# Kernel tuning notes

Hardware: AMD Instinct MI355X
Metric: run time of the kernel (lower is better)

The kernel has to match this reference:

```python
import jax, jax.numpy as jnp
import numpy as np

N_NODES = 50000
N_EDGES = 1250000
IN_CH = 64
HID = 64
N_CLASSES = 10
N_GRAPHS = 128


def _xavier(key, shape):
    fan_out, fan_in = shape
    limit = np.sqrt(6.0 / (fan_in + fan_out))
    return jax.random.uniform(key, shape, jnp.float32, -limit, limit)


def setup_inputs() -> dict:
    key = jax.random.key(0)
    ks = jax.random.split(key, 12)
    x = jax.random.normal(ks[0], (N_NODES, IN_CH), jnp.float32)
    edge_index = jax.random.randint(ks[1], (2, N_EDGES), 0, N_NODES, jnp.int64)
    batch = jnp.sort(jax.random.randint(ks[2], (N_NODES,), 0, N_GRAPHS, jnp.int64))
    return {
        "x": x,
        "edge_index": edge_index,
        "batch": batch,
        # GraphConv i: lin_rel (weight+bias) applied to aggregated neighbors,
        # lin_root (no bias) applied to self features. Weights are [out, in].
        "W1_rel": _xavier(ks[3], (HID, IN_CH)), "b1": jnp.zeros((HID,), jnp.float32),
        "W1_root": _xavier(ks[4], (HID, IN_CH)),
        "W2_rel": _xavier(ks[5], (HID, HID)), "b2": jnp.zeros((HID,), jnp.float32),
        "W2_root": _xavier(ks[6], (HID, HID)),
        "W3_rel": _xavier(ks[7], (HID, HID)), "b3": jnp.zeros((HID,), jnp.float32),
        "W3_root": _xavier(ks[8], (HID, HID)),
        "W_lin": _xavier(ks[9], (N_CLASSES, HID)), "b_lin": jnp.zeros((N_CLASSES,), jnp.float32),
    }


def _graph_conv(x, src, dst, W_rel, b, W_root):
    # sum-aggregate neighbor features: gather at src, scatter-add at dst
    agg = jax.ops.segment_sum(x[src], dst, num_segments=N_NODES)  # [N, F]
    return agg @ W_rel.T + b + x @ W_root.T


def reference(x, edge_index, batch, W1_rel, b1, W1_root, W2_rel, b2, W2_root,
              W3_rel, b3, W3_root, W_lin, b_lin):
    src, dst = edge_index[0], edge_index[1]
    h = jax.nn.relu(_graph_conv(x, src, dst, W1_rel, b1, W1_root))
    h = jax.nn.relu(_graph_conv(h, src, dst, W2_rel, b2, W2_root))
    h = _graph_conv(h, src, dst, W3_rel, b3, W3_root)
    # global mean pool over graphs
    sums = jax.ops.segment_sum(h, batch, num_segments=N_GRAPHS)        # [G, HID]
    counts = jax.ops.segment_sum(jnp.ones((h.shape[0],), h.dtype), batch,
                                 num_segments=N_GRAPHS)
    pooled = sums / jnp.maximum(counts, 1.0)[:, None]
    out = pooled @ W_lin.T + b_lin  # dropout inactive in eval mode
    return (pooled, out)
```

## Files before the change

kernel.cpp:

```cpp
#include <hip/hip_runtime.h>

#define N_NODES   50000
#define HID       64
#define N_GRAPHS  128
#define N_CLASSES 10
#define NP        196
#define EPA       8192
#define PCAP      8192

typedef __attribute__((ext_vector_type(8))) short short8;
typedef __attribute__((ext_vector_type(4))) float f32x4;

__device__ __forceinline__ unsigned bf16rne(float f) {
    unsigned u = __float_as_uint(f);
    return (u + 0x7fffu + ((u >> 16) & 1u)) >> 16;
}
__device__ __forceinline__ unsigned pack_bf16x2(float lo, float hi) {
    return bf16rne(lo) | (bf16rne(hi) << 16);
}



__global__ void cvt_kernel(const float* __restrict__ x, unsigned short* __restrict__ xb,
                           int* __restrict__ gcursor) {
    if (blockIdx.x == 0 && threadIdx.x < NP) gcursor[threadIdx.x] = 0;
    int i = blockIdx.x * blockDim.x + threadIdx.x;
    if (i < N_NODES * 16) {
        float4 v = ((const float4*)x)[i];
        uint2 o;
        o.x = pack_bf16x2(v.x, v.y);
        o.y = pack_bf16x2(v.z, v.w);
        ((uint2*)xb)[i] = o;
    }
}


__global__ __launch_bounds__(256) void bucket_kernel(
    const int* __restrict__ src, const int* __restrict__ dst,
    int* __restrict__ gcursor, unsigned* __restrict__ packed, int E) {
    __shared__ int hist[NP], scp[NP], base[NP], cnt2[NP];
    __shared__ int sc[256];
    __shared__ unsigned stag[EPA];
    const int t = threadIdx.x;
    const int e0 = blockIdx.x * EPA;
    const int e1 = min(e0 + EPA, E);
    for (int i = t; i < NP; i += 256) { hist[i] = 0; cnt2[i] = 0; }
    __syncthreads();
    for (int e = e0 + t; e < e1; e += 256)
        atomicAdd(&hist[dst[e] >> 8], 1);
    __syncthreads();
    sc[t] = (t < NP) ? hist[t] : 0;
    __syncthreads();
    for (int off = 1; off < 256; off <<= 1) {
        int add = (t >= off) ? sc[t - off] : 0;
        __syncthreads();
        sc[t] += add;
        __syncthreads();
    }
    if (t < NP) {
        scp[t] = sc[t] - hist[t];
        if (hist[t] > 0) base[t] = atomicAdd(&gcursor[t], hist[t]);
    }
    __syncthreads();
    for (int e = e0 + t; e < e1; e += 256) {
        int d = dst[e], s = src[e];
        int p = d >> 8;
        int idx = scp[p] + atomicAdd(&cnt2[p], 1);
        stag[idx] = (unsigned)s | ((unsigned)(d & 255) << 16) | ((unsigned)p << 24);
    }
    __syncthreads();
    const int n = e1 - e0;
    for (int i = t; i < n; i += 256) {
        unsigned v = stag[i];
        int p = v >> 24;
        packed[(size_t)p * PCAP + base[p] + (i - scp[p])] = v & 0x00FFFFFFu;
    }
}

__global__ __launch_bounds__(256) void build_kernel(
    const unsigned* __restrict__ packed, const int* __restrict__ gcursor,
    int* __restrict__ offsets, unsigned short* __restrict__ csr,
    int* __restrict__ sums_zero) {
    __shared__ int hist[256], lofs[256], cnt[256], sc[256], gv[256];
    __shared__ unsigned short lcsr[PCAP];
    const int p = blockIdx.x, t = threadIdx.x;

    if (p == 0) {
        for (int i = t; i < N_GRAPHS * 64; i += 256) sums_zero[i] = 0;
    }

    int v = (t < NP) ? gcursor[t] : 0;
    sc[t] = v; gv[t] = v;
    __syncthreads();
    for (int off = 1; off < 256; off <<= 1) {
        int add = (t >= off) ? sc[t - off] : 0;
        __syncthreads();
        sc[t] += add;
        __syncthreads();
    }
    const int pb = sc[p] - gv[p];
    const int ne = gv[p];
    if (p == NP - 1 && t == 0) offsets[N_NODES] = sc[NP - 1];
    __syncthreads();

    const unsigned* mypk = packed + (size_t)p * PCAP;
    hist[t] = 0; cnt[t] = 0;
    __syncthreads();
    for (int i = t; i < ne; i += 256)
        atomicAdd(&hist[(mypk[i] >> 16) & 255], 1);
    __syncthreads();
    sc[t] = hist[t];
    __syncthreads();
    for (int off = 1; off < 256; off <<= 1) {
        int add = (t >= off) ? sc[t - off] : 0;
        __syncthreads();
        sc[t] += add;
        __syncthreads();
    }
    lofs[t] = sc[t] - hist[t];
    int node = p * 256 + t;
    if (node < N_NODES) offsets[node] = pb + lofs[t];
    __syncthreads();
    for (int i = t; i < ne; i += 256) {
        unsigned vv = mypk[i];
        int dl = (vv >> 16) & 255;
        int slot = lofs[dl] + atomicAdd(&cnt[dl], 1);
        lcsr[slot] = (unsigned short)(vv & 0xFFFFu);
    }
    __syncthreads();
    for (int i = t; i < ne; i += 256) csr[pb + i] = lcsr[i];
}


__global__ __launch_bounds__(256) void gather_kernel(
    const unsigned short* __restrict__ hin,
    const int* __restrict__ offsets, const unsigned short* __restrict__ csr_src,
    unsigned short* __restrict__ agg) {
    const int w = threadIdx.x >> 6, lane = threadIdx.x & 63;
    const int rg = lane >> 3;
    const int cg = lane & 7;
    const int n = blockIdx.x * 4 + w;
    const int beg = offsets[n], end = offsets[n + 1];

    float acc[8] = {0.f, 0.f, 0.f, 0.f, 0.f, 0.f, 0.f, 0.f};
    for (int base = beg; base < end; base += 64) {
        int cnt = min(64, end - base);
        int sidx = (base + lane < end) ? (int)csr_src[base + lane] : 0;
        for (int kb = 0; kb < cnt; kb += 32) {
            uint4 u[4];
#pragma unroll
            for (int p = 0; p < 4; ++p) {
                int e = kb + 8 * p + rg;
                int r = __shfl(sidx, e);
                if (e < cnt)
                    u[p] = *((const uint4*)(hin + (size_t)r * 64) + cg);
                else
                    u[p] = make_uint4(0u, 0u, 0u, 0u);
            }
#pragma unroll
            for (int p = 0; p < 4; ++p) {
                acc[0] += __uint_as_float(u[p].x << 16);
                acc[1] += __uint_as_float(u[p].x & 0xffff0000u);
                acc[2] += __uint_as_float(u[p].y << 16);
                acc[3] += __uint_as_float(u[p].y & 0xffff0000u);
                acc[4] += __uint_as_float(u[p].z << 16);
                acc[5] += __uint_as_float(u[p].z & 0xffff0000u);
                acc[6] += __uint_as_float(u[p].w << 16);
                acc[7] += __uint_as_float(u[p].w & 0xffff0000u);
            }
        }
    }
#pragma unroll
    for (int m = 8; m <= 32; m <<= 1)
#pragma unroll
        for (int j = 0; j < 8; ++j)
            acc[j] += __shfl_xor(acc[j], m);
    if (rg == 0) {
        uint4 o;
        o.x = pack_bf16x2(acc[0], acc[1]);
        o.y = pack_bf16x2(acc[2], acc[3]);
        o.z = pack_bf16x2(acc[4], acc[5]);
        o.w = pack_bf16x2(acc[6], acc[7]);
        *((uint4*)(agg + (size_t)n * 64) + cg) = o;
    }
}


template <int RELU, int POOL>
__global__ __launch_bounds__(256) void linear_kernel(
    const unsigned short* __restrict__ agg,
    const unsigned short* __restrict__ hin,
    const float* __restrict__ Wrel, const float* __restrict__ bias,
    const float* __restrict__ Wroot, unsigned short* __restrict__ hout,
    const int* __restrict__ batch, float* __restrict__ sums) {
    const int tid = threadIdx.x;
    const int w = tid >> 6, lane = tid & 63;
    const int q = lane >> 4, c = lane & 15;
    const int g0 = (blockIdx.x * 4 + w) * 16;
    if (g0 >= N_NODES) return;

    short8 brel[4][2], broot[4][2];
    float biasv[4];
#pragma unroll
    for (int t = 0; t < 4; ++t) {
        int o = t * 16 + c;
        biasv[t] = bias[o];
#pragma unroll
        for (int s = 0; s < 2; ++s) {
            const float4* pr = (const float4*)(Wrel  + o * 64 + s * 32 + q * 8);
            const float4* po = (const float4*)(Wroot + o * 64 + s * 32 + q * 8);
            float4 r0 = pr[0], r1 = pr[1], z0 = po[0], z1 = po[1];
            short8 rr, zz;
            rr[0] = (short)bf16rne(r0.x); rr[1] = (short)bf16rne(r0.y);
            rr[2] = (short)bf16rne(r0.z); rr[3] = (short)bf16rne(r0.w);
            rr[4] = (short)bf16rne(r1.x); rr[5] = (short)bf16rne(r1.y);
            rr[6] = (short)bf16rne(r1.z); rr[7] = (short)bf16rne(r1.w);
            zz[0] = (short)bf16rne(z0.x); zz[1] = (short)bf16rne(z0.y);
            zz[2] = (short)bf16rne(z0.z); zz[3] = (short)bf16rne(z0.w);
            zz[4] = (short)bf16rne(z1.x); zz[5] = (short)bf16rne(z1.y);
            zz[6] = (short)bf16rne(z1.z); zz[7] = (short)bf16rne(z1.w);
            brel[t][s] = rr; broot[t][s] = zz;
        }
    }

    const int na = min(g0 + c, N_NODES - 1);
    short8 a_agg[2], a_x[2];
#pragma unroll
    for (int s = 0; s < 2; ++s) {
        a_agg[s] = *(const short8*)(agg + (size_t)na * 64 + s * 32 + q * 8);
        a_x[s]   = *(const short8*)(hin + (size_t)na * 64 + s * 32 + q * 8);
    }

    f32x4 acc4[4];
#pragma unroll
    for (int t = 0; t < 4; ++t) {
        f32x4 a0 = {biasv[t], biasv[t], biasv[t], biasv[t]};
        a0 = __builtin_amdgcn_mfma_f32_16x16x32_bf16(a_agg[0], brel[t][0], a0, 0, 0, 0);
        a0 = __builtin_amdgcn_mfma_f32_16x16x32_bf16(a_agg[1], brel[t][1], a0, 0, 0, 0);
        a0 = __builtin_amdgcn_mfma_f32_16x16x32_bf16(a_x[0],  broot[t][0], a0, 0, 0, 0);
        a0 = __builtin_amdgcn_mfma_f32_16x16x32_bf16(a_x[1],  broot[t][1], a0, 0, 0, 0);
        acc4[t] = a0;
    }

    if (POOL) {
        int b0 = batch[g0], b15 = batch[g0 + 15];
        if (b0 == b15) {
#pragma unroll
            for (int t = 0; t < 4; ++t) {
                float s = acc4[t][0] + acc4[t][1] + acc4[t][2] + acc4[t][3];
                s += __shfl_xor(s, 16);
                s += __shfl_xor(s, 32);
                if (q == 0) atomicAdd(&sums[b0 * 64 + t * 16 + c], s);
            }
        } else {
#pragma unroll
            for (int r = 0; r < 4; ++r) {
                int bq = batch[g0 + q * 4 + r];
#pragma unroll
                for (int t = 0; t < 4; ++t)
                    atomicAdd(&sums[bq * 64 + t * 16 + c], acc4[t][r]);
            }
        }
    } else {
        __shared__ unsigned short outT[4][16][72];
#pragma unroll
        for (int t = 0; t < 4; ++t)
#pragma unroll
            for (int r = 0; r < 4; ++r) {
                float v = acc4[t][r];
                if (RELU) v = fmaxf(v, 0.f);
                outT[w][q * 4 + r][t * 16 + c] = (unsigned short)bf16rne(v);
            }
#pragma unroll
        for (int it = 0; it < 2; ++it) {
            int row = it * 8 + (lane >> 3);
            int ch = (lane & 7) * 8;
            int n = g0 + row;
            if (n < N_NODES) {
                short8 v = *(const short8*)&outT[w][row][ch];
                *(short8*)(hout + (size_t)n * 64 + ch) = v;
            }
        }
    }
}


__global__ void final_kernel(const float* __restrict__ sums, const int* __restrict__ batch,
                             const float* __restrict__ Wlin, const float* __restrict__ blin,
                             float* __restrict__ out) {
    __shared__ float pl[64];
    int g = blockIdx.x, lane = threadIdx.x;
    int lo = 0, hi = N_NODES;
    while (lo < hi) { int m = (lo + hi) >> 1; if (batch[m] < g) lo = m + 1; else hi = m; }
    int s0 = lo;
    lo = 0; hi = N_NODES;
    while (lo < hi) { int m = (lo + hi) >> 1; if (batch[m] < g + 1) lo = m + 1; else hi = m; }
    float cdiv = fmaxf((float)(lo - s0), 1.0f);
    float p = sums[g * 64 + lane] / cdiv;
    out[g * 64 + lane] = p;
    pl[lane] = p;
    __syncthreads();
    if (lane < N_CLASSES) {
        float o = blin[lane];
#pragma unroll
        for (int k = 0; k < 64; ++k) o += pl[k] * Wlin[lane * 64 + k];
        out[N_GRAPHS * 64 + g * N_CLASSES + lane] = o;
    }
}


extern "C" void kernel_launch(void* const* d_in, const int* in_sizes, int n_in,
                              void* d_out, int out_size, void* d_ws, size_t ws_size,
                              hipStream_t stream) {
    const float* x     = (const float*)d_in[0];
    const int*   ei    = (const int*)d_in[1];
    const int*   batch = (const int*)d_in[2];
    const float* W1r = (const float*)d_in[3];
    const float* b1  = (const float*)d_in[4];
    const float* W1o = (const float*)d_in[5];
    const float* W2r = (const float*)d_in[6];
    const float* b2  = (const float*)d_in[7];
    const float* W2o = (const float*)d_in[8];
    const float* W3r = (const float*)d_in[9];
    const float* b3  = (const float*)d_in[10];
    const float* W3o = (const float*)d_in[11];
    const float* Wl  = (const float*)d_in[12];
    const float* bl  = (const float*)d_in[13];
    float* out = (float*)d_out;

    const int E = in_sizes[1] / 2;
    const int* src = ei;
    const int* dst = ei + E;

    char* p = (char*)d_ws;
    unsigned short* xb  = (unsigned short*)p; p += (size_t)N_NODES * 64 * 2;
    unsigned short* h1  = (unsigned short*)p; p += (size_t)N_NODES * 64 * 2;
    unsigned short* h2  = (unsigned short*)p; p += (size_t)N_NODES * 64 * 2;
    unsigned short* agg = (unsigned short*)p; p += (size_t)N_NODES * 64 * 2;
    unsigned* packed    = (unsigned*)p; p += (size_t)NP * PCAP * 4;
    unsigned short* csr = (unsigned short*)p; p += (size_t)E * 2;
    int* offsets   = (int*)p;   p += (size_t)(N_NODES + 1) * 4;
    int* gcursor   = (int*)p;   p += NP * 4;
    float* sums    = (float*)p; p += (size_t)N_GRAPHS * 64 * 4;

    const int NCHUNK = (E + EPA - 1) / EPA;
    cvt_kernel<<<(N_NODES * 16 + 255) / 256, 256, 0, stream>>>(x, xb, gcursor);
    bucket_kernel<<<NCHUNK, 256, 0, stream>>>(src, dst, gcursor, packed, E);
    build_kernel<<<NP, 256, 0, stream>>>(packed, gcursor, offsets, csr, (int*)sums);

    const int GB = N_NODES / 4;
    const int LB = (N_NODES + 63) / 64;
    gather_kernel<<<GB, 256, 0, stream>>>(xb, offsets, csr, agg);
    linear_kernel<1, 0><<<LB, 256, 0, stream>>>(agg, xb, W1r, b1, W1o, h1, batch, sums);
    gather_kernel<<<GB, 256, 0, stream>>>(h1, offsets, csr, agg);
    linear_kernel<1, 0><<<LB, 256, 0, stream>>>(agg, h1, W2r, b2, W2o, h2, batch, sums);
    gather_kernel<<<GB, 256, 0, stream>>>(h2, offsets, csr, agg);
    linear_kernel<0, 1><<<LB, 256, 0, stream>>>(agg, h2, W3r, b3, W3o, h1, batch, sums);

    final_kernel<<<N_GRAPHS, 64, 0, stream>>>(sums, batch, Wl, bl, out);
}
```

Before: 263.0 us.

## Process two nodes per wavefront in gather and precompute graph boundaries

The gather kernel now assigns two consecutive nodes to each 64-lane wavefront, with each half-wave loading up to 32 neighbour indices per node and issuing eight row loads per iteration instead of four. This is meant to give more memory-level parallelism and less per-node loop overhead, since average degree is about 25 and many lanes sat idle. Graph start offsets are also computed once in the convert kernel, replacing two binary searches per graph in the final kernel. The cost is higher register pressure from two accumulator sets, and the two nodes' loops run together, so they take as long as the higher-degree one.

```diff
diff --git a/kernel.cpp b/kernel.cpp
--- a/kernel.cpp
+++ b/kernel.cpp
@@ -22,9 +22,17 @@
 
 
 __global__ void cvt_kernel(const float* __restrict__ x, unsigned short* __restrict__ xb,
-                           int* __restrict__ gcursor) {
+                           int* __restrict__ gcursor, const int* __restrict__ batch,
+                           int* __restrict__ gstart) {
+    int i = blockIdx.x * blockDim.x + threadIdx.x;
     if (blockIdx.x == 0 && threadIdx.x < NP) gcursor[threadIdx.x] = 0;
-    int i = blockIdx.x * blockDim.x + threadIdx.x;
+    if (i < N_NODES) {
+        int b = batch[i];
+        int bp = (i > 0) ? batch[i - 1] : -1;
+        for (int g = bp + 1; g <= b; ++g) gstart[g] = i;
+        if (i == N_NODES - 1)
+            for (int g = b + 1; g <= N_GRAPHS; ++g) gstart[g] = N_NODES;
+    }
     if (i < N_NODES * 16) {
         float4 v = ((const float4*)x)[i];
         uint2 o;
@@ -139,49 +147,77 @@
     const int w = threadIdx.x >> 6, lane = threadIdx.x & 63;
     const int rg = lane >> 3;
     const int cg = lane & 7;
-    const int n = blockIdx.x * 4 + w;
-    const int beg = offsets[n], end = offsets[n + 1];
-
-    float acc[8] = {0.f, 0.f, 0.f, 0.f, 0.f, 0.f, 0.f, 0.f};
-    for (int base = beg; base < end; base += 64) {
-        int cnt = min(64, end - base);
-        int sidx = (base + lane < end) ? (int)csr_src[base + lane] : 0;
-        for (int kb = 0; kb < cnt; kb += 32) {
-            uint4 u[4];
-#pragma unroll
-            for (int p = 0; p < 4; ++p) {
-                int e = kb + 8 * p + rg;
-                int r = __shfl(sidx, e);
-                if (e < cnt)
-                    u[p] = *((const uint4*)(hin + (size_t)r * 64) + cg);
-                else
-                    u[p] = make_uint4(0u, 0u, 0u, 0u);
-            }
-#pragma unroll
-            for (int p = 0; p < 4; ++p) {
-                acc[0] += __uint_as_float(u[p].x << 16);
-                acc[1] += __uint_as_float(u[p].x & 0xffff0000u);
-                acc[2] += __uint_as_float(u[p].y << 16);
-                acc[3] += __uint_as_float(u[p].y & 0xffff0000u);
-                acc[4] += __uint_as_float(u[p].z << 16);
-                acc[5] += __uint_as_float(u[p].z & 0xffff0000u);
-                acc[6] += __uint_as_float(u[p].w << 16);
-                acc[7] += __uint_as_float(u[p].w & 0xffff0000u);
-            }
-        }
+    const int n0 = (blockIdx.x * 4 + w) * 2;
+    const int begA = offsets[n0];
+    const int endA = offsets[n0 + 1];
+    const int endB = offsets[n0 + 2];
+
+    float accA[8] = {0.f,0.f,0.f,0.f,0.f,0.f,0.f,0.f};
+    float accB[8] = {0.f,0.f,0.f,0.f,0.f,0.f,0.f,0.f};
+    int eA = begA, eB = endA;
+    while (eA < endA || eB < endB) {
+        int cntA = endA - eA; cntA = (cntA > 32) ? 32 : cntA;
+        int cntB = endB - eB; cntB = (cntB > 32) ? 32 : cntB;
+        int idx;
+        if (lane < 32) idx = (lane < cntA) ? (int)csr_src[eA + lane] : 0;
+        else           idx = ((lane - 32) < cntB) ? (int)csr_src[eB + (lane - 32)] : 0;
+        uint4 uA[4], uB[4];
+#pragma unroll
+        for (int p = 0; p < 4; ++p) {
+            int e = 8 * p + rg;
+            int rA = __shfl(idx, e);
+            uA[p] = (e < cntA) ? *((const uint4*)(hin + (size_t)rA * 64) + cg)
+                               : make_uint4(0u, 0u, 0u, 0u);
+        }
+#pragma unroll
+        for (int p = 0; p < 4; ++p) {
+            int e = 8 * p + rg;
+            int rB = __shfl(idx, 32 + e);
+            uB[p] = (e < cntB) ? *((const uint4*)(hin + (size_t)rB * 64) + cg)
+                               : make_uint4(0u, 0u, 0u, 0u);
+        }
+#pragma unroll
+        for (int p = 0; p < 4; ++p) {
+            accA[0] += __uint_as_float(uA[p].x << 16);
+            accA[1] += __uint_as_float(uA[p].x & 0xffff0000u);
+            accA[2] += __uint_as_float(uA[p].y << 16);
+            accA[3] += __uint_as_float(uA[p].y & 0xffff0000u);
+            accA[4] += __uint_as_float(uA[p].z << 16);
+            accA[5] += __uint_as_float(uA[p].z & 0xffff0000u);
+            accA[6] += __uint_as_float(uA[p].w << 16);
+            accA[7] += __uint_as_float(uA[p].w & 0xffff0000u);
+            accB[0] += __uint_as_float(uB[p].x << 16);
+            accB[1] += __uint_as_float(uB[p].x & 0xffff0000u);
+            accB[2] += __uint_as_float(uB[p].y << 16);
+            accB[3] += __uint_as_float(uB[p].y & 0xffff0000u);
+            accB[4] += __uint_as_float(uB[p].z << 16);
+            accB[5] += __uint_as_float(uB[p].z & 0xffff0000u);
+            accB[6] += __uint_as_float(uB[p].w << 16);
+            accB[7] += __uint_as_float(uB[p].w & 0xffff0000u);
+        }
+        eA += cntA; eB += cntB;
     }
 #pragma unroll
     for (int m = 8; m <= 32; m <<= 1)
 #pragma unroll
-        for (int j = 0; j < 8; ++j)
-            acc[j] += __shfl_xor(acc[j], m);
+        for (int j = 0; j < 8; ++j) {
+            accA[j] += __shfl_xor(accA[j], m);
+            accB[j] += __shfl_xor(accB[j], m);
+        }
     if (rg == 0) {
         uint4 o;
-        o.x = pack_bf16x2(acc[0], acc[1]);
-        o.y = pack_bf16x2(acc[2], acc[3]);
-        o.z = pack_bf16x2(acc[4], acc[5]);
-        o.w = pack_bf16x2(acc[6], acc[7]);
-        *((uint4*)(agg + (size_t)n * 64) + cg) = o;
+        o.x = pack_bf16x2(accA[0], accA[1]);
+        o.y = pack_bf16x2(accA[2], accA[3]);
+        o.z = pack_bf16x2(accA[4], accA[5]);
+        o.w = pack_bf16x2(accA[6], accA[7]);
+        *((uint4*)(agg + (size_t)n0 * 64) + cg) = o;
+    } else if (rg == 1) {
+        uint4 o;
+        o.x = pack_bf16x2(accB[0], accB[1]);
+        o.y = pack_bf16x2(accB[2], accB[3]);
+        o.z = pack_bf16x2(accB[4], accB[5]);
+        o.w = pack_bf16x2(accB[6], accB[7]);
+        *((uint4*)(agg + (size_t)(n0 + 1) * 64) + cg) = o;
     }
 }
 
@@ -285,17 +321,12 @@
 }
 
 
-__global__ void final_kernel(const float* __restrict__ sums, const int* __restrict__ batch,
+__global__ void final_kernel(const float* __restrict__ sums, const int* __restrict__ gstart,
                              const float* __restrict__ Wlin, const float* __restrict__ blin,
                              float* __restrict__ out) {
     __shared__ float pl[64];
     int g = blockIdx.x, lane = threadIdx.x;
-    int lo = 0, hi = N_NODES;
-    while (lo < hi) { int m = (lo + hi) >> 1; if (batch[m] < g) lo = m + 1; else hi = m; }
-    int s0 = lo;
-    lo = 0; hi = N_NODES;
-    while (lo < hi) { int m = (lo + hi) >> 1; if (batch[m] < g + 1) lo = m + 1; else hi = m; }
-    float cdiv = fmaxf((float)(lo - s0), 1.0f);
+    float cdiv = fmaxf((float)(gstart[g + 1] - gstart[g]), 1.0f);
     float p = sums[g * 64 + lane] / cdiv;
     out[g * 64 + lane] = p;
     pl[lane] = p;
@@ -342,13 +373,14 @@
     int* offsets   = (int*)p;   p += (size_t)(N_NODES + 1) * 4;
     int* gcursor   = (int*)p;   p += NP * 4;
     float* sums    = (float*)p; p += (size_t)N_GRAPHS * 64 * 4;
+    int* gstart    = (int*)p;   p += (N_GRAPHS + 1) * 4;
 
     const int NCHUNK = (E + EPA - 1) / EPA;
-    cvt_kernel<<<(N_NODES * 16 + 255) / 256, 256, 0, stream>>>(x, xb, gcursor);
+    cvt_kernel<<<(N_NODES * 16 + 255) / 256, 256, 0, stream>>>(x, xb, gcursor, batch, gstart);
     bucket_kernel<<<NCHUNK, 256, 0, stream>>>(src, dst, gcursor, packed, E);
     build_kernel<<<NP, 256, 0, stream>>>(packed, gcursor, offsets, csr, (int*)sums);
 
-    const int GB = N_NODES / 4;
+    const int GB = N_NODES / 8;
     const int LB = (N_NODES + 63) / 64;
     gather_kernel<<<GB, 256, 0, stream>>>(xb, offsets, csr, agg);
     linear_kernel<1, 0><<<LB, 256, 0, stream>>>(agg, xb, W1r, b1, W1o, h1, batch, sums);
@@ -357,5 +389,5 @@
     gather_kernel<<<GB, 256, 0, stream>>>(h2, offsets, csr, agg);
     linear_kernel<0, 1><<<LB, 256, 0, stream>>>(agg, h2, W3r, b3, W3o, h1, batch, sums);
 
-    final_kernel<<<N_GRAPHS, 64, 0, stream>>>(sums, batch, Wl, bl, out);
-}
+    final_kernel<<<N_GRAPHS, 64, 0, stream>>>(sums, gstart, Wl, bl, out);
+}
```

After: 273.1 us. 3.8% more time.

## Fuse neighbor gather and linear transform into one per-layer kernel

Applied to the files above, without the earlier changes.

Merges the gather and linear kernels into one layer kernel. Each wave aggregates 16 nodes sequentially into LDS, then runs the MFMA transform using bf16 weight fragments staged once per block in shared memory. This removes the global agg round trip and three launches. It also precomputes graph start indices in the convert kernel so the final kernel skips binary searches. The cost is fewer waves in flight during the gather: one wave per 16 nodes, against one per node before. That may hurt latency hiding for the irregular loads.

```diff
diff --git a/kernel.cpp b/kernel.cpp
--- a/kernel.cpp
+++ b/kernel.cpp
@@ -22,9 +22,17 @@
 
 
 __global__ void cvt_kernel(const float* __restrict__ x, unsigned short* __restrict__ xb,
-                           int* __restrict__ gcursor) {
+                           int* __restrict__ gcursor, const int* __restrict__ batch,
+                           int* __restrict__ gstart) {
+    int i = blockIdx.x * blockDim.x + threadIdx.x;
     if (blockIdx.x == 0 && threadIdx.x < NP) gcursor[threadIdx.x] = 0;
-    int i = blockIdx.x * blockDim.x + threadIdx.x;
+    if (i < N_NODES) {
+        int b = batch[i];
+        int bp = (i > 0) ? batch[i - 1] : -1;
+        for (int g = bp + 1; g <= b; ++g) gstart[g] = i;
+        if (i == N_NODES - 1)
+            for (int g = b + 1; g <= N_GRAPHS; ++g) gstart[g] = N_NODES;
+    }
     if (i < N_NODES * 16) {
         float4 v = ((const float4*)x)[i];
         uint2 o;
@@ -132,113 +140,105 @@
 }
 
 
-__global__ __launch_bounds__(256) void gather_kernel(
+template <int RELU, int POOL>
+__global__ __launch_bounds__(256) void layer_kernel(
     const unsigned short* __restrict__ hin,
     const int* __restrict__ offsets, const unsigned short* __restrict__ csr_src,
-    unsigned short* __restrict__ agg) {
-    const int w = threadIdx.x >> 6, lane = threadIdx.x & 63;
-    const int rg = lane >> 3;
-    const int cg = lane & 7;
-    const int n = blockIdx.x * 4 + w;
-    const int beg = offsets[n], end = offsets[n + 1];
-
-    float acc[8] = {0.f, 0.f, 0.f, 0.f, 0.f, 0.f, 0.f, 0.f};
-    for (int base = beg; base < end; base += 64) {
-        int cnt = min(64, end - base);
-        int sidx = (base + lane < end) ? (int)csr_src[base + lane] : 0;
-        for (int kb = 0; kb < cnt; kb += 32) {
-            uint4 u[4];
-#pragma unroll
-            for (int p = 0; p < 4; ++p) {
-                int e = kb + 8 * p + rg;
-                int r = __shfl(sidx, e);
-                if (e < cnt)
-                    u[p] = *((const uint4*)(hin + (size_t)r * 64) + cg);
-                else
-                    u[p] = make_uint4(0u, 0u, 0u, 0u);
-            }
-#pragma unroll
-            for (int p = 0; p < 4; ++p) {
-                acc[0] += __uint_as_float(u[p].x << 16);
-                acc[1] += __uint_as_float(u[p].x & 0xffff0000u);
-                acc[2] += __uint_as_float(u[p].y << 16);
-                acc[3] += __uint_as_float(u[p].y & 0xffff0000u);
-                acc[4] += __uint_as_float(u[p].z << 16);
-                acc[5] += __uint_as_float(u[p].z & 0xffff0000u);
-                acc[6] += __uint_as_float(u[p].w << 16);
-                acc[7] += __uint_as_float(u[p].w & 0xffff0000u);
-            }
-        }
-    }
-#pragma unroll
-    for (int m = 8; m <= 32; m <<= 1)
-#pragma unroll
-        for (int j = 0; j < 8; ++j)
-            acc[j] += __shfl_xor(acc[j], m);
-    if (rg == 0) {
-        uint4 o;
-        o.x = pack_bf16x2(acc[0], acc[1]);
-        o.y = pack_bf16x2(acc[2], acc[3]);
-        o.z = pack_bf16x2(acc[4], acc[5]);
-        o.w = pack_bf16x2(acc[6], acc[7]);
-        *((uint4*)(agg + (size_t)n * 64) + cg) = o;
-    }
-}
-
-
-template <int RELU, int POOL>
-__global__ __launch_bounds__(256) void linear_kernel(
-    const unsigned short* __restrict__ agg,
-    const unsigned short* __restrict__ hin,
     const float* __restrict__ Wrel, const float* __restrict__ bias,
     const float* __restrict__ Wroot, unsigned short* __restrict__ hout,
     const int* __restrict__ batch, float* __restrict__ sums) {
+    __shared__ short8 wfrag[2][4][2][4][16];
+    __shared__ unsigned short agg_lds[64][72];
+
     const int tid = threadIdx.x;
     const int w = tid >> 6, lane = tid & 63;
+    const int g0 = (blockIdx.x * 4 + w) * 16;
+
+    for (int f = tid; f < 1024; f += 256) {
+        int m = f >> 9;
+        int r = f & 511;
+        int t = r >> 7, s = (r >> 6) & 1, q = (r >> 4) & 3, c = r & 15;
+        const float* W = m ? Wroot : Wrel;
+        const float4* pw = (const float4*)(W + (t * 16 + c) * 64 + s * 32 + q * 8);
+        float4 v0 = pw[0], v1 = pw[1];
+        short8 fr;
+        fr[0] = (short)bf16rne(v0.x); fr[1] = (short)bf16rne(v0.y);
+        fr[2] = (short)bf16rne(v0.z); fr[3] = (short)bf16rne(v0.w);
+        fr[4] = (short)bf16rne(v1.x); fr[5] = (short)bf16rne(v1.y);
+        fr[6] = (short)bf16rne(v1.z); fr[7] = (short)bf16rne(v1.w);
+        wfrag[m][t][s][q][c] = fr;
+    }
+
+    if (g0 < N_NODES) {
+        const int rg = lane >> 3;
+        const int cg = lane & 7;
+        int myoff = (lane < 17) ? offsets[g0 + lane] : 0;
+        for (int i = 0; i < 16; ++i) {
+            const int beg = __shfl(myoff, i), end = __shfl(myoff, i + 1);
+            float acc[8] = {0.f, 0.f, 0.f, 0.f, 0.f, 0.f, 0.f, 0.f};
+            for (int base = beg; base < end; base += 64) {
+                int cnt = min(64, end - base);
+                int sidx = (base + lane < end) ? (int)csr_src[base + lane] : 0;
+                for (int kb = 0; kb < cnt; kb += 32) {
+                    uint4 u[4];
+#pragma unroll
+                    for (int p = 0; p < 4; ++p) {
+                        int e = kb + 8 * p + rg;
+                        int r = __shfl(sidx, e);
+                        u[p] = (e < cnt) ? *((const uint4*)(hin + (size_t)r * 64) + cg)
+                                         : make_uint4(0u, 0u, 0u, 0u);
+                    }
+#pragma unroll
+                    for (int p = 0; p < 4; ++p) {
+                        acc[0] += __uint_as_float(u[p].x << 16);
+                        acc[1] += __uint_as_float(u[p].x & 0xffff0000u);
+                        acc[2] += __uint_as_float(u[p].y << 16);
+                        acc[3] += __uint_as_float(u[p].y & 0xffff0000u);
+                        acc[4] += __uint_as_float(u[p].z << 16);
+                        acc[5] += __uint_as_float(u[p].z & 0xffff0000u);
+                        acc[6] += __uint_as_float(u[p].w << 16);
+                        acc[7] += __uint_as_float(u[p].w & 0xffff0000u);
+                    }
+                }
+            }
+#pragma unroll
+            for (int m = 8; m <= 32; m <<= 1)
+#pragma unroll
+                for (int j = 0; j < 8; ++j)
+                    acc[j] += __shfl_xor(acc[j], m);
+            if (rg == 0) {
+                uint4 o;
+                o.x = pack_bf16x2(acc[0], acc[1]);
+                o.y = pack_bf16x2(acc[2], acc[3]);
+                o.z = pack_bf16x2(acc[4], acc[5]);
+                o.w = pack_bf16x2(acc[6], acc[7]);
+                *((uint4*)&agg_lds[w * 16 + i][cg * 8]) = o;
+            }
+        }
+    }
+
+    __syncthreads();
+    if (g0 >= N_NODES) return;
+
     const int q = lane >> 4, c = lane & 15;
-    const int g0 = (blockIdx.x * 4 + w) * 16;
-    if (g0 >= N_NODES) return;
-
-    short8 brel[4][2], broot[4][2];
+    short8 a_agg[2], a_x[2];
+#pragma unroll
+    for (int s = 0; s < 2; ++s) {
+        a_agg[s] = *(const short8*)&agg_lds[w * 16 + c][s * 32 + q * 8];
+        a_x[s]   = *(const short8*)(hin + (size_t)(g0 + c) * 64 + s * 32 + q * 8);
+    }
     float biasv[4];
 #pragma unroll
-    for (int t = 0; t < 4; ++t) {
-        int o = t * 16 + c;
-        biasv[t] = bias[o];
-#pragma unroll
-        for (int s = 0; s < 2; ++s) {
-            const float4* pr = (const float4*)(Wrel  + o * 64 + s * 32 + q * 8);
-            const float4* po = (const float4*)(Wroot + o * 64 + s * 32 + q * 8);
-            float4 r0 = pr[0], r1 = pr[1], z0 = po[0], z1 = po[1];
-            short8 rr, zz;
-            rr[0] = (short)bf16rne(r0.x); rr[1] = (short)bf16rne(r0.y);
-            rr[2] = (short)bf16rne(r0.z); rr[3] = (short)bf16rne(r0.w);
-            rr[4] = (short)bf16rne(r1.x); rr[5] = (short)bf16rne(r1.y);
-            rr[6] = (short)bf16rne(r1.z); rr[7] = (short)bf16rne(r1.w);
-            zz[0] = (short)bf16rne(z0.x); zz[1] = (short)bf16rne(z0.y);
-            zz[2] = (short)bf16rne(z0.z); zz[3] = (short)bf16rne(z0.w);
-            zz[4] = (short)bf16rne(z1.x); zz[5] = (short)bf16rne(z1.y);
-            zz[6] = (short)bf16rne(z1.z); zz[7] = (short)bf16rne(z1.w);
-            brel[t][s] = rr; broot[t][s] = zz;
-        }
-    }
-
-    const int na = min(g0 + c, N_NODES - 1);
-    short8 a_agg[2], a_x[2];
-#pragma unroll
-    for (int s = 0; s < 2; ++s) {
-        a_agg[s] = *(const short8*)(agg + (size_t)na * 64 + s * 32 + q * 8);
-        a_x[s]   = *(const short8*)(hin + (size_t)na * 64 + s * 32 + q * 8);
-    }
+    for (int t = 0; t < 4; ++t) biasv[t] = bias[t * 16 + c];
 
     f32x4 acc4[4];
 #pragma unroll
     for (int t = 0; t < 4; ++t) {
         f32x4 a0 = {biasv[t], biasv[t], biasv[t], biasv[t]};
-        a0 = __builtin_amdgcn_mfma_f32_16x16x32_bf16(a_agg[0], brel[t][0], a0, 0, 0, 0);
-        a0 = __builtin_amdgcn_mfma_f32_16x16x32_bf16(a_agg[1], brel[t][1], a0, 0, 0, 0);
-        a0 = __builtin_amdgcn_mfma_f32_16x16x32_bf16(a_x[0],  broot[t][0], a0, 0, 0, 0);
-        a0 = __builtin_amdgcn_mfma_f32_16x16x32_bf16(a_x[1],  broot[t][1], a0, 0, 0, 0);
+        a0 = __builtin_amdgcn_mfma_f32_16x16x32_bf16(a_agg[0], wfrag[0][t][0][q][c], a0, 0, 0, 0);
+        a0 = __builtin_amdgcn_mfma_f32_16x16x32_bf16(a_agg[1], wfrag[0][t][1][q][c], a0, 0, 0, 0);
+        a0 = __builtin_amdgcn_mfma_f32_16x16x32_bf16(a_x[0],   wfrag[1][t][0][q][c], a0, 0, 0, 0);
+        a0 = __builtin_amdgcn_mfma_f32_16x16x32_bf16(a_x[1],   wfrag[1][t][1][q][c], a0, 0, 0, 0);
         acc4[t] = a0;
     }
 
@@ -262,40 +262,31 @@
             }
         }
     } else {
-        __shared__ unsigned short outT[4][16][72];
 #pragma unroll
         for (int t = 0; t < 4; ++t)
 #pragma unroll
             for (int r = 0; r < 4; ++r) {
                 float v = acc4[t][r];
                 if (RELU) v = fmaxf(v, 0.f);
-                outT[w][q * 4 + r][t * 16 + c] = (unsigned short)bf16rne(v);
+                agg_lds[w * 16 + q * 4 + r][t * 16 + c] = (unsigned short)bf16rne(v);
             }
 #pragma unroll
         for (int it = 0; it < 2; ++it) {
             int row = it * 8 + (lane >> 3);
             int ch = (lane & 7) * 8;
-            int n = g0 + row;
-            if (n < N_NODES) {
-                short8 v = *(const short8*)&outT[w][row][ch];
-                *(short8*)(hout + (size_t)n * 64 + ch) = v;
-            }
+            short8 v = *(const short8*)&agg_lds[w * 16 + row][ch];
+            *(short8*)(hout + (size_t)(g0 + row) * 64 + ch) = v;
         }
     }
 }
 
 
-__global__ void final_kernel(const float* __restrict__ sums, const int* __restrict__ batch,
+__global__ void final_kernel(const float* __restrict__ sums, const int* __restrict__ gstart,
                              const float* __restrict__ Wlin, const float* __restrict__ blin,
                              float* __restrict__ out) {
     __shared__ float pl[64];
     int g = blockIdx.x, lane = threadIdx.x;
-    int lo = 0, hi = N_NODES;
-    while (lo < hi) { int m = (lo + hi) >> 1; if (batch[m] < g) lo = m + 1; else hi = m; }
-    int s0 = lo;
-    lo = 0; hi = N_NODES;
-    while (lo < hi) { int m = (lo + hi) >> 1; if (batch[m] < g + 1) lo = m + 1; else hi = m; }
-    float cdiv = fmaxf((float)(lo - s0), 1.0f);
+    float cdiv = fmaxf((float)(gstart[g + 1] - gstart[g]), 1.0f);
     float p = sums[g * 64 + lane] / cdiv;
     out[g * 64 + lane] = p;
     pl[lane] = p;
@@ -336,26 +327,22 @@
     unsigned short* xb  = (unsigned short*)p; p += (size_t)N_NODES * 64 * 2;
     unsigned short* h1  = (unsigned short*)p; p += (size_t)N_NODES * 64 * 2;
     unsigned short* h2  = (unsigned short*)p; p += (size_t)N_NODES * 64 * 2;
-    unsigned short* agg = (unsigned short*)p; p += (size_t)N_NODES * 64 * 2;
     unsigned* packed    = (unsigned*)p; p += (size_t)NP * PCAP * 4;
     unsigned short* csr = (unsigned short*)p; p += (size_t)E * 2;
     int* offsets   = (int*)p;   p += (size_t)(N_NODES + 1) * 4;
     int* gcursor   = (int*)p;   p += NP * 4;
     float* sums    = (float*)p; p += (size_t)N_GRAPHS * 64 * 4;
+    int* gstart    = (int*)p;   p += (N_GRAPHS + 1) * 4;
 
     const int NCHUNK = (E + EPA - 1) / EPA;
-    cvt_kernel<<<(N_NODES * 16 + 255) / 256, 256, 0, stream>>>(x, xb, gcursor);
+    cvt_kernel<<<(N_NODES * 16 + 255) / 256, 256, 0, stream>>>(x, xb, gcursor, batch, gstart);
     bucket_kernel<<<NCHUNK, 256, 0, stream>>>(src, dst, gcursor, packed, E);
     build_kernel<<<NP, 256, 0, stream>>>(packed, gcursor, offsets, csr, (int*)sums);
 
-    const int GB = N_NODES / 4;
     const int LB = (N_NODES + 63) / 64;
-    gather_kernel<<<GB, 256, 0, stream>>>(xb, offsets, csr, agg);
-    linear_kernel<1, 0><<<LB, 256, 0, stream>>>(agg, xb, W1r, b1, W1o, h1, batch, sums);
-    gather_kernel<<<GB, 256, 0, stream>>>(h1, offsets, csr, agg);
-    linear_kernel<1, 0><<<LB, 256, 0, stream>>>(agg, h1, W2r, b2, W2o, h2, batch, sums);
-    gather_kernel<<<GB, 256, 0, stream>>>(h2, offsets, csr, agg);
-    linear_kernel<0, 1><<<LB, 256, 0, stream>>>(agg, h2, W3r, b3, W3o, h1, batch, sums);
-
-    final_kernel<<<N_GRAPHS, 64, 0, stream>>>(sums, batch, Wl, bl, out);
-}
+    layer_kernel<1, 0><<<LB, 256, 0, stream>>>(xb, offsets, csr, W1r, b1, W1o, h1, batch, sums);
+    layer_kernel<1, 0><<<LB, 256, 0, stream>>>(h1, offsets, csr, W2r, b2, W2o, h2, batch, sums);
+    layer_kernel<0, 1><<<LB, 256, 0, stream>>>(h2, offsets, csr, W3r, b3, W3o, h1, batch, sums);
+
+    final_kernel<<<N_GRAPHS, 64, 0, stream>>>(sums, gstart, Wl, bl, out);
+}
```

Measured after the change: 250.8 us. 4.7% less time.
